# Kernel optimization log

Hardware: AMD Instinct MI355X
Metric: run time of the kernel (lower is better)

Reference implementation:

```python
import jax, jax.numpy as jnp
import numpy as np

# Longformer-base-4096 dims; attention_window=128 -> one-sided window 64
B, S, D, H, L, F, V, NUM_LABELS = 1, 4096, 768, 12, 12, 3072, 50265, 100
DH = D // H
W = 64            # one-sided sliding window
NC = S // W       # number of query chunks
EPS = 1e-5
SCALE = float(1.0 / np.sqrt(DH))


def layer_norm(x, s, b):
    m = jnp.mean(x, axis=-1, keepdims=True)
    v = jnp.mean(jnp.square(x - m), axis=-1, keepdims=True)
    return (x - m) * jax.lax.rsqrt(v + EPS) * s + b


def heads(x):  # [B,S,D] -> [B,H,S,DH]
    return x.reshape(B, S, H, DH).transpose(0, 2, 1, 3)


def chunk3(t):  # [B,H,S,DH] -> [B,H,NC,3W,DH]: key blocks c-1,c,c+1 per query chunk c
    tp = jnp.pad(t, ((0, 0), (0, 0), (W, W), (0, 0)))
    tb = tp.reshape(B, H, NC + 2, W, DH)
    return jnp.concatenate([tb[:, :, i:i + NC] for i in range(3)], axis=3)


def _forward(input_ids, attention_mask, emb_tok, emb_pos, ln_emb_scale, ln_emb_bias,
             Wq, bq, Wk, bk, Wv, bv, Wqg, bqg, Wkg, bkg, Wvg, bvg, Wo, bo,
             ln1_scale, ln1_bias, Wf1, bf1, Wf2, bf2, ln2_scale, ln2_bias, Wc, bc):
    am = attention_mask > 0                      # [B,S]
    x = layer_norm(emb_tok[input_ids] + emb_pos[None, :, :], ln_emb_scale, ln_emb_bias)

    # static sliding-window masks, shared by all layers
    qi = jnp.arange(W)[:, None]
    kj = jnp.arange(3 * W)[None, :]
    band = (kj >= qi) & (kj <= qi + 2 * W)       # |key - query| <= W within a chunk triple
    kvalid = am & (jnp.arange(S)[None, :] > 0)   # global token (pos 0) excluded from window
    kp = jnp.pad(kvalid, ((0, 0), (W, W))).reshape(B, NC + 2, W)
    kmask = jnp.concatenate([kp[:, i:i + NC] for i in range(3)], axis=2)   # [B,NC,3W]
    win_mask = band[None, None, None] & kmask[:, None, :, None, :]         # [B,1,NC,W,3W]

    def layer(x, p):
        (wq, bq_, wk, bk_, wv, bv_, wqg, bqg_, wkg, bkg_, wvg, bvg_, wo, bo_,
         l1s, l1b, wf1, bf1_, wf2, bf2_, l2s, l2b) = p
        q = heads(x @ wq + bq_) * SCALE
        k = heads(x @ wk + bk_)
        v = heads(x @ wv + bv_)
        qc = q.reshape(B, H, NC, W, DH)
        k3, v3 = chunk3(k), chunk3(v)
        sc = jnp.einsum('bhcqd,bhckd->bhcqk', qc, k3)          # [B,H,NC,W,3W]
        sc = jnp.where(win_mask, sc, -1e9)
        # every token also attends to the global CLS key (standard K/V of pos 0)
        sg = jnp.einsum('bhsd,bhd->bhs', q, k[:, :, 0]).reshape(B, H, NC, W, 1)
        probs = jax.nn.softmax(jnp.concatenate([sg, sc], axis=-1), axis=-1)
        pg, pl = probs[..., 0], probs[..., 1:]
        ctx = jnp.einsum('bhcqk,bhckd->bhcqd', pl, v3).reshape(B, H, S, DH)
        ctx = ctx + pg.reshape(B, H, S, 1) * v[:, :, :1]
        # global token attends to everything with its own (global) projections
        qg = heads(x @ wqg + bqg_)[:, :, 0] * SCALE            # [B,H,DH]
        kg = heads(x @ wkg + bkg_)
        vg = heads(x @ wvg + bvg_)
        sgl = jnp.where(am[:, None, :], jnp.einsum('bhd,bhjd->bhj', qg, kg), -1e9)
        ctx0 = jnp.einsum('bhj,bhjd->bhd', jax.nn.softmax(sgl, axis=-1), vg)
        ctx = ctx.at[:, :, 0].set(ctx0)
        attn = ctx.transpose(0, 2, 1, 3).reshape(B, S, D) @ wo + bo_
        x1 = layer_norm(x + attn, l1s, l1b)
        h = jax.nn.gelu(x1 @ wf1 + bf1_, approximate=False)
        return layer_norm(x1 + h @ wf2 + bf2_, l2s, l2b), None

    params = (Wq, bq, Wk, bk, Wv, bv, Wqg, bqg, Wkg, bkg, Wvg, bvg, Wo, bo,
              ln1_scale, ln1_bias, Wf1, bf1, Wf2, bf2, ln2_scale, ln2_bias)
    x, _ = jax.lax.scan(layer, x, params)
    return x[:, 0] @ Wc + bc                                   # [B, NUM_LABELS]


def setup_inputs():
    key = jax.random.key(0)
    ks = jax.random.split(key, 40)
    it = iter(range(40))
    nrm = lambda shape: jax.random.normal(ks[next(it)], shape, dtype=jnp.float32) * 0.02
    z = lambda shape: jnp.zeros(shape, jnp.float32)
    o = lambda shape: jnp.ones(shape, jnp.float32)
    return {
        'input_ids': jax.random.randint(ks[next(it)], (B, S), 0, V, dtype=jnp.int32),
        'attention_mask': jnp.ones((B, S), dtype=jnp.int32),
        'emb_tok': nrm((V, D)), 'emb_pos': nrm((S, D)),
        'ln_emb_scale': o((D,)), 'ln_emb_bias': z((D,)),
        'Wq': nrm((L, D, D)), 'bq': z((L, D)),
        'Wk': nrm((L, D, D)), 'bk': z((L, D)),
        'Wv': nrm((L, D, D)), 'bv': z((L, D)),
        'Wqg': nrm((L, D, D)), 'bqg': z((L, D)),
        'Wkg': nrm((L, D, D)), 'bkg': z((L, D)),
        'Wvg': nrm((L, D, D)), 'bvg': z((L, D)),
        'Wo': nrm((L, D, D)), 'bo': z((L, D)),
        'ln1_scale': o((L, D)), 'ln1_bias': z((L, D)),
        'Wf1': nrm((L, D, F)), 'bf1': z((L, F)),
        'Wf2': nrm((L, F, D)), 'bf2': z((L, D)),
        'ln2_scale': o((L, D)), 'ln2_bias': z((L, D)),
        'Wc': nrm((D, NUM_LABELS)), 'bc': z((NUM_LABELS,)),
    }


def reference(input_ids, attention_mask, emb_tok, emb_pos, ln_emb_scale, ln_emb_bias,
              Wq, bq, Wk, bk, Wv, bv, Wqg, bqg, Wkg, bkg, Wvg, bvg, Wo, bo,
              ln1_scale, ln1_bias, Wf1, bf1, Wf2, bf2, ln2_scale, ln2_bias, Wc, bc):
    return _forward(input_ids, attention_mask, emb_tok, emb_pos, ln_emb_scale, ln_emb_bias,
                    Wq, bq, Wk, bk, Wv, bv, Wqg, bqg, Wkg, bkg, Wvg, bvg, Wo, bo,
                    ln1_scale, ln1_bias, Wf1, bf1, Wf2, bf2, ln2_scale, ln2_bias, Wc, bc)
```

## Files before the change

### kernel.cpp

```cpp
#include <hip/hip_runtime.h>
#include <hip/hip_bf16.h>

typedef unsigned short u16;
typedef __attribute__((ext_vector_type(8))) short bf16x8;
typedef __attribute__((ext_vector_type(4))) float f32x4;

constexpr int S = 4096, D = 768, H = 12, NL = 12, F = 3072, NLAB = 100, DH = 64;
constexpr int NQKV = 3840;
constexpr float SCALE = 0.125f;
constexpr float EPS = 1e-5f;

__device__ __forceinline__ float bits2f(u16 u) {
  union { unsigned int i; float f; } x; x.i = ((unsigned int)u) << 16; return x.f;
}
__device__ __forceinline__ u16 f2bbits(float f) {
  union { float f; unsigned int i; } x; x.f = f;
  return (u16)((x.i + 0x7FFFu + ((x.i >> 16) & 1u)) >> 16);
}
__device__ __forceinline__ float rdw(const void* p, size_t i, int isf32) {
  return isf32 ? ((const float*)p)[i] : bits2f(((const u16*)p)[i]);
}
__device__ __forceinline__ void gload16(const void* g, void* l) {
  __builtin_amdgcn_global_load_lds(
      (const __attribute__((address_space(1))) void*)g,
      (__attribute__((address_space(3))) void*)l, 16, 0, 0);
}

__global__ void detect_k(const void* lns, int* flag) {
  *flag = (*(const unsigned int*)lns == 0x3F800000u) ? 1 : 0;
}

struct PrepArgs {
  const void *Wq, *Wk, *Wv, *Wkg, *Wvg, *Wo, *Wqg, *Wf1, *Wf2;
  const void *bq, *bk, *bv, *bkg, *bvg, *bo, *bqg, *bf1, *bf2;
  size_t oDD, oDF, oD, oF;
  u16 *wt_qkv, *wt_o, *wt_qg, *wt_f1, *wt_f2;
  float* biasb;
  const int* flag;
};

__global__ __launch_bounds__(256) void prep_layer(PrepArgs a)
{
  const int b = blockIdx.x, t = threadIdx.x;
  const int isf32 = *a.flag;
  if (b < 8640) {
    __shared__ float tile[32][33];
    const void* src; size_t soff; int N, ld, rowoff, n0, k0;
    u16* dst; float scl = 1.f;
    if (b < 4032) {
      const int m = b / 576, ti = b - m * 576;
      soff = a.oDD; N = D; ld = D; rowoff = 0;
      switch (m) {
        case 0:  src = a.Wq;  dst = a.wt_qkv; scl = SCALE;  break;
        case 1:  src = a.Wk;  dst = a.wt_qkv; rowoff = 768; break;
        case 2:  src = a.Wv;  dst = a.wt_qkv; rowoff = 1536; break;
        case 3:  src = a.Wkg; dst = a.wt_qkv; rowoff = 2304; break;
        case 4:  src = a.Wvg; dst = a.wt_qkv; rowoff = 3072; break;
        case 5:  src = a.Wo;  dst = a.wt_o;   break;
        default: src = a.Wqg; dst = a.wt_qg;  scl = SCALE;  break;
      }
      n0 = (ti % 24) * 32; k0 = (ti / 24) * 32;
    } else if (b < 6336) {
      const int ti = b - 4032;
      src = a.Wf1; soff = a.oDF; N = F; dst = a.wt_f1; rowoff = 0; ld = D;
      n0 = (ti % 96) * 32; k0 = (ti / 96) * 32;
    } else {
      const int ti = b - 6336;
      src = a.Wf2; soff = a.oDF; N = D; dst = a.wt_f2; rowoff = 0; ld = F;
      n0 = (ti % 24) * 32; k0 = (ti / 24) * 32;
    }
    const int r = t >> 3, cc = (t & 7) << 2;
    const size_t si = soff + (size_t)(k0 + r) * N + n0 + cc;
    if (isf32) {
      const float4 v = *reinterpret_cast<const float4*>(&((const float*)src)[si]);
      tile[r][cc] = v.x * scl; tile[r][cc+1] = v.y * scl;
      tile[r][cc+2] = v.z * scl; tile[r][cc+3] = v.w * scl;
    } else {
      const ushort4 v = *reinterpret_cast<const ushort4*>(&((const u16*)src)[si]);
      tile[r][cc] = bits2f(v.x) * scl; tile[r][cc+1] = bits2f(v.y) * scl;
      tile[r][cc+2] = bits2f(v.z) * scl; tile[r][cc+3] = bits2f(v.w) * scl;
    }
    __syncthreads();
    const ushort4 ov = make_ushort4(f2bbits(tile[cc+0][r]), f2bbits(tile[cc+1][r]),
                                    f2bbits(tile[cc+2][r]), f2bbits(tile[cc+3][r]));
    *reinterpret_cast<ushort4*>(&dst[(size_t)(rowoff + n0 + r) * ld + k0 + cc]) = ov;
  } else {
    const int i = (b - 8640) * 256 + t;
    float v;
    if      (i < 768)  v = rdw(a.bq,  a.oD + i,        isf32) * SCALE;
    else if (i < 1536) v = rdw(a.bk,  a.oD + i - 768,  isf32);
    else if (i < 2304) v = rdw(a.bv,  a.oD + i - 1536, isf32);
    else if (i < 3072) v = rdw(a.bkg, a.oD + i - 2304, isf32);
    else if (i < 3840) v = rdw(a.bvg, a.oD + i - 3072, isf32);
    else if (i < 4608) v = rdw(a.bo,  a.oD + i - 3840, isf32);
    else if (i < 7680) v = rdw(a.bf1, a.oF + i - 4608, isf32);
    else if (i < 8448) v = rdw(a.bf2, a.oD + i - 7680, isf32);
    else               v = rdw(a.bqg, a.oD + i - 8448, isf32) * SCALE;
    a.biasb[i] = v;
  }
}

template<int BN, int SPLITK>
__global__ __launch_bounds__(256) void mfma_gemm(
    const u16* __restrict__ A, const u16* __restrict__ BT,
    const float* __restrict__ bias,
    float* __restrict__ Cf, u16* __restrict__ Cb,
    int M, int N, int K, int act)
{
  constexpr int BM = 128, BK = 32;
  constexpr int WN = BN / 2;
  constexpr int NR = WN / 16;
  __shared__ u16 As[BM * BK];
  __shared__ u16 Bs[BN * BK];
  const int t = threadIdx.x;
  const int wid = t >> 6, lane = t & 63;
  const int wr = wid >> 1, wc = wid & 1;
  const int m0 = blockIdx.y * BM, n0 = blockIdx.x * BN;
  const int z = (SPLITK > 1) ? blockIdx.z : 0;
  const int kLen = K / SPLITK;
  const int k0 = z * kLen;
  const int l_row = lane >> 2;
  const int l_kc = (lane & 3) << 3;

  f32x4 acc[4][NR];
#pragma unroll
  for (int m = 0; m < 4; ++m)
#pragma unroll
    for (int n = 0; n < NR; ++n)
      acc[m][n] = (f32x4){0.f, 0.f, 0.f, 0.f};

  const int frow = lane & 15;
  const int fkb = (lane >> 4) << 3;

  for (int kt = k0; kt < k0 + kLen; kt += BK) {
#pragma unroll
    for (int i = 0; i < 2; ++i) {
      const int ch = wid * 2 + i;
      gload16(&A[(size_t)(m0 + ch * 16 + l_row) * K + kt + l_kc], &As[ch * 512]);
    }
#pragma unroll
    for (int i = 0; i < BN / 64; ++i) {
      const int ch = wid * (BN / 64) + i;
      gload16(&BT[(size_t)(n0 + ch * 16 + l_row) * K + kt + l_kc], &Bs[ch * 512]);
    }
    __syncthreads();
    bf16x8 af[4], bfr[NR];
#pragma unroll
    for (int m = 0; m < 4; ++m)
      af[m] = *reinterpret_cast<const bf16x8*>(&As[(wr * 64 + m * 16 + frow) * BK + fkb]);
#pragma unroll
    for (int n = 0; n < NR; ++n)
      bfr[n] = *reinterpret_cast<const bf16x8*>(&Bs[(wc * WN + n * 16 + frow) * BK + fkb]);
#pragma unroll
    for (int m = 0; m < 4; ++m)
#pragma unroll
      for (int n = 0; n < NR; ++n)
        acc[m][n] = __builtin_amdgcn_mfma_f32_16x16x32_bf16(af[m], bfr[n], acc[m][n], 0, 0, 0);
    __syncthreads();
  }

  float* Cp = (SPLITK > 1) ? (Cf + (size_t)z * M * N) : Cf;
  const int crow = (lane >> 4) << 2;
  const int ccol = lane & 15;
#pragma unroll
  for (int m = 0; m < 4; ++m) {
#pragma unroll
    for (int n = 0; n < NR; ++n) {
      const int gc = n0 + wc * WN + n * 16 + ccol;
      const float bv = (z == 0) ? bias[gc] : 0.f;
#pragma unroll
      for (int r = 0; r < 4; ++r) {
        const int gr = m0 + wr * 64 + m * 16 + crow + r;
        float x = acc[m][n][r] + bv;
        if (SPLITK == 1 && act) x = 0.5f * x * (1.0f + erff(x * 0.70710678118654752f));
        if (Cp) Cp[(size_t)gr * N + gc] = x;
        if (SPLITK == 1 && Cb) Cb[(size_t)gr * N + gc] = f2bbits(x);
      }
    }
  }
}

__global__ void embed_k(const int* __restrict__ ids, const void* __restrict__ tok,
                        const void* __restrict__ pos, float* __restrict__ out,
                        const int* __restrict__ flag)
{
  const int isf32 = *flag;
  const int s = blockIdx.x, t = threadIdx.x;
  const int id = ids[s];
  for (int c = t; c < D; c += 256)
    out[(size_t)s * D + c] = rdw(tok, (size_t)id * D + c, isf32) + rdw(pos, (size_t)s * D + c, isf32);
}

__global__ __launch_bounds__(256) void ln_res_k(
    const float* __restrict__ Ain,
    const float* __restrict__ P0, const float* __restrict__ P1,
    const float* __restrict__ P2, const float* __restrict__ P3,
    const void* __restrict__ g, size_t goff, const void* __restrict__ b, size_t boff,
    float* __restrict__ Out, u16* __restrict__ Outb, const int* __restrict__ flag)
{
  __shared__ float buf[D];
  __shared__ float red[4];
  const int isf32 = *flag;
  const int r = blockIdx.x, t = threadIdx.x;
  float ls = 0.f;
  for (int c = t; c < D; c += 256) {
    const size_t i = (size_t)r * D + c;
    float v = Ain[i];
    if (P0) v += P0[i];
    if (P1) v += P1[i];
    if (P2) v += P2[i];
    if (P3) v += P3[i];
    buf[c] = v; ls += v;
  }
#pragma unroll
  for (int off = 32; off; off >>= 1) ls += __shfl_xor(ls, off);
  if ((t & 63) == 0) red[t >> 6] = ls;
  __syncthreads();
  const float mean = (red[0] + red[1] + red[2] + red[3]) * (1.0f / D);
  __syncthreads();
  float lv = 0.f;
  for (int c = t; c < D; c += 256) { const float dd = buf[c] - mean; lv += dd * dd; }
#pragma unroll
  for (int off = 32; off; off >>= 1) lv += __shfl_xor(lv, off);
  if ((t & 63) == 0) red[t >> 6] = lv;
  __syncthreads();
  const float var = (red[0] + red[1] + red[2] + red[3]) * (1.0f / D);
  const float rstd = rsqrtf(var + EPS);
  for (int c = t; c < D; c += 256) {
    const float o = (buf[c] - mean) * rstd * rdw(g, goff + c, isf32) + rdw(b, boff + c, isf32);
    Out[(size_t)r * D + c] = o;
    if (Outb) Outb[(size_t)r * D + c] = f2bbits(o);
  }
}

__global__ __launch_bounds__(256) void qg_gemv(
    const u16* __restrict__ Xb, const u16* __restrict__ WgT,
    const float* __restrict__ biasb, float* __restrict__ QG)
{
  const int wid = threadIdx.x >> 6, lane = threadIdx.x & 63;
  const int o = blockIdx.x * 4 + wid;
  float a = 0.f;
#pragma unroll
  for (int j = 0; j < 12; ++j) {
    const int k = j * 64 + lane;
    a += bits2f(Xb[k]) * bits2f(WgT[(size_t)o * 768 + k]);
  }
#pragma unroll
  for (int off = 32; off; off >>= 1) a += __shfl_xor(a, off);
  if (lane == 0) QG[o] = a + biasb[8448 + o];
}

__global__ __launch_bounds__(256) void win_attn3(
    const u16* __restrict__ QKV, const int* __restrict__ am, u16* __restrict__ CTXb)
{
  __shared__ u16 Ql[64 * 64];
  __shared__ u16 Kl[224 * 64];
  __shared__ u16 Vt[64 * 232];
  __shared__ int kwin[224];
  const int c = blockIdx.x, h = blockIdx.y;
  const int t = threadIdx.x, w = t >> 6, lane = t & 63;
  const int base = c * 64 - 64, s0 = c * 64;

  for (int i = t; i < 1024; i += 256) {
    const int r = i >> 4, c4 = (i & 15) << 2;
    const ushort4 v = *reinterpret_cast<const ushort4*>(
        &QKV[(size_t)(s0 + r) * NQKV + h * 64 + c4]);
    *reinterpret_cast<ushort4*>((char*)Ql + ((r * 128 + c4 * 2) ^ ((r & 7) << 4))) = v;
  }
  for (int i = t; i < 3584; i += 256) {
    const int r = i >> 4, c4 = (i & 15) << 2;
    const int kp = (r < 192) ? (base + r) : ((r == 192) ? 0 : -1);
    ushort4 v = make_ushort4(0, 0, 0, 0);
    if (kp >= 0 && kp < S)
      v = *reinterpret_cast<const ushort4*>(&QKV[(size_t)kp * NQKV + 768 + h * 64 + c4]);
    *reinterpret_cast<ushort4*>((char*)Kl + ((r * 128 + c4 * 2) ^ ((r & 7) << 4))) = v;
  }
  for (int i = t; i < 3584; i += 256) {
    const int r = i >> 4, c4 = (i & 15) << 2;
    const int kp = (r < 192) ? (base + r) : ((r == 192) ? 0 : -1);
    ushort4 v = make_ushort4(0, 0, 0, 0);
    if (kp >= 0 && kp < S)
      v = *reinterpret_cast<const ushort4*>(&QKV[(size_t)kp * NQKV + 1536 + h * 64 + c4]);
    Vt[(c4 + 0) * 232 + r] = v.x;
    Vt[(c4 + 1) * 232 + r] = v.y;
    Vt[(c4 + 2) * 232 + r] = v.z;
    Vt[(c4 + 3) * 232 + r] = v.w;
  }
  if (t < 224) {
    const int kp = base + t;
    kwin[t] = (t < 192 && kp >= 1 && kp < S) ? am[kp] : 0;
  }
  __syncthreads();

  const int frow = lane & 15, fkb = (lane >> 4) << 3;
  const int crow = (lane >> 4) << 2, ccol = lane & 15;
  const int qrow = w * 16 + frow;

  bf16x8 aq[2];
#pragma unroll
  for (int ks = 0; ks < 2; ++ks)
    aq[ks] = *reinterpret_cast<const bf16x8*>(
        (const char*)Ql + ((qrow * 128 + (ks * 32 + fkb) * 2) ^ ((qrow & 7) << 4)));

  f32x4 sc[14];
#pragma unroll
  for (int tl = 0; tl < 14; ++tl) {
    sc[tl] = (f32x4){0.f, 0.f, 0.f, 0.f};
    const int key = tl * 16 + frow;
#pragma unroll
    for (int ks = 0; ks < 2; ++ks) {
      const bf16x8 bk = *reinterpret_cast<const bf16x8*>(
          (const char*)Kl + ((key * 128 + (ks * 32 + fkb) * 2) ^ ((key & 7) << 4)));
      sc[tl] = __builtin_amdgcn_mfma_f32_16x16x32_bf16(aq[ks], bk, sc[tl], 0, 0, 0);
    }
  }

  float m4[4] = {-1e30f, -1e30f, -1e30f, -1e30f};
#pragma unroll
  for (int tl = 0; tl < 14; ++tl) {
    const int kidx = tl * 16 + ccol;
    const int kw = kwin[kidx];
    const bool isg = (kidx == 192);
#pragma unroll
    for (int r = 0; r < 4; ++r) {
      const int qi = w * 16 + crow + r;
      const bool valid = isg || ((kidx >= qi) && (kidx <= qi + 128) && kw);
      const float v = valid ? sc[tl][r] : -1e30f;
      sc[tl][r] = v;
      m4[r] = fmaxf(m4[r], v);
    }
  }
#pragma unroll
  for (int r = 0; r < 4; ++r)
#pragma unroll
    for (int off = 8; off; off >>= 1) m4[r] = fmaxf(m4[r], __shfl_xor(m4[r], off));

  float ssum[4] = {0.f, 0.f, 0.f, 0.f};
#pragma unroll
  for (int tl = 0; tl < 14; ++tl)
#pragma unroll
    for (int r = 0; r < 4; ++r) {
      const float e = __expf(sc[tl][r] - m4[r]);
      sc[tl][r] = e;
      ssum[r] += e;
    }
#pragma unroll
  for (int r = 0; r < 4; ++r)
#pragma unroll
    for (int off = 8; off; off >>= 1) ssum[r] += __shfl_xor(ssum[r], off);

  __syncthreads();
  u16* Pl = Kl;
#pragma unroll
  for (int tl = 0; tl < 14; ++tl) {
    const int kidx = tl * 16 + ccol;
#pragma unroll
    for (int r = 0; r < 4; ++r) {
      const int row = crow + r;
      *(u16*)((char*)Pl + w * 7168 + ((row * 448 + kidx * 2) ^ ((row & 7) << 4))) =
          f2bbits(sc[tl][r]);
    }
  }
  __syncthreads();

  bf16x8 pa[7];
#pragma unroll
  for (int ks = 0; ks < 7; ++ks)
    pa[ks] = *reinterpret_cast<const bf16x8*>(
        (const char*)Pl + w * 7168 + ((frow * 448 + (ks * 32 + fkb) * 2) ^ ((frow & 7) << 4)));

  f32x4 av[4];
#pragma unroll
  for (int n = 0; n < 4; ++n) {
    av[n] = (f32x4){0.f, 0.f, 0.f, 0.f};
#pragma unroll
    for (int ks = 0; ks < 7; ++ks) {
      const bf16x8 bv = *reinterpret_cast<const bf16x8*>(&Vt[(n * 16 + frow) * 232 + ks * 32 + fkb]);
      av[n] = __builtin_amdgcn_mfma_f32_16x16x32_bf16(pa[ks], bv, av[n], 0, 0, 0);
    }
  }
  float inv[4];
#pragma unroll
  for (int r = 0; r < 4; ++r) inv[r] = 1.f / ssum[r];
#pragma unroll
  for (int n = 0; n < 4; ++n)
#pragma unroll
    for (int r = 0; r < 4; ++r) {
      const int s = s0 + w * 16 + crow + r;
      CTXb[(size_t)s * D + h * 64 + n * 16 + ccol] = f2bbits(av[n][r] * inv[r]);
    }
}

__global__ __launch_bounds__(256) void glob_part(
    const u16* __restrict__ QKV, const float* __restrict__ QG,
    const int* __restrict__ am, float* __restrict__ gp)
{
  __shared__ float qsh[DH];
  __shared__ float se[256];
  __shared__ float red[4];
  __shared__ float part[4][DH];
  const int seg = blockIdx.x, h = blockIdx.y, t = threadIdx.x;
  const int j0 = seg * 256;
  if (t < DH) qsh[t] = QG[h * DH + t];
  __syncthreads();
  const int j = j0 + t;
  float a = 0.f;
  const u16* kr = &QKV[(size_t)j * NQKV + 2304 + h * 64];
#pragma unroll
  for (int v8 = 0; v8 < 8; ++v8) {
    const bf16x8 kv = *reinterpret_cast<const bf16x8*>(&kr[v8 * 8]);
#pragma unroll
    for (int e = 0; e < 8; ++e)
      a += qsh[v8 * 8 + e] * bits2f((u16)kv[e]);
  }
  a = (am[j] > 0) ? a : -1e9f;
  float m = a;
#pragma unroll
  for (int off = 32; off; off >>= 1) m = fmaxf(m, __shfl_xor(m, off));
  if ((t & 63) == 0) red[t >> 6] = m;
  __syncthreads();
  m = fmaxf(fmaxf(red[0], red[1]), fmaxf(red[2], red[3]));
  const float e = __expf(a - m);
  se[t] = e;
  float ls = e;
#pragma unroll
  for (int off = 32; off; off >>= 1) ls += __shfl_xor(ls, off);
  __syncthreads();
  if ((t & 63) == 0) red[t >> 6] = ls;
  __syncthreads();
  const float lsum = red[0] + red[1] + red[2] + red[3];
  const int g = t >> 6, d = t & 63;
  float acc = 0.f;
  for (int jj = g; jj < 256; jj += 4)
    acc += se[jj] * bits2f(QKV[(size_t)(j0 + jj) * NQKV + 3072 + h * 64 + d]);
  part[g][d] = acc;
  __syncthreads();
  if (t < 64) {
    float* o = &gp[(size_t)(h * 16 + seg) * 66];
    o[t] = part[0][t] + part[1][t] + part[2][t] + part[3][t];
    if (t == 0) { o[64] = m; o[65] = lsum; }
  }
}

__global__ void glob_comb(const float* __restrict__ gp, u16* __restrict__ CTXb)
{
  const int h = blockIdx.x, t = threadIdx.x;
  float M = -1e30f;
  for (int i = 0; i < 16; ++i) M = fmaxf(M, gp[(size_t)(h * 16 + i) * 66 + 64]);
  float L = 0.f, acc = 0.f;
  for (int i = 0; i < 16; ++i) {
    const float* o = &gp[(size_t)(h * 16 + i) * 66];
    const float w = __expf(o[64] - M);
    L += o[65] * w;
    acc += o[t] * w;
  }
  CTXb[h * 64 + t] = f2bbits(acc / L);
}

__global__ __launch_bounds__(256) void cls_k(
    const float* __restrict__ X, const void* __restrict__ Wc,
    const void* __restrict__ bc, void* __restrict__ out,
    const int* __restrict__ flag)
{
  const int isf32 = *flag;
  const int wid = threadIdx.x >> 6, lane = threadIdx.x & 63;
  const int n = blockIdx.x * 4 + wid;
  if (n >= NLAB) return;
  float a = 0.f;
#pragma unroll
  for (int j = 0; j < 12; ++j) {
    const int k = j * 64 + lane;
    a += X[k] * rdw(Wc, (size_t)k * NLAB + n, isf32);
  }
#pragma unroll
  for (int off = 32; off; off >>= 1) a += __shfl_xor(a, off);
  if (lane == 0) {
    a += rdw(bc, n, isf32);
    if (isf32) ((float*)out)[n] = a;
    else ((u16*)out)[n] = f2bbits(a);
  }
}

extern "C" void kernel_launch(void* const* d_in, const int* in_sizes, int n_in,
                              void* d_out, int out_size, void* d_ws, size_t ws_size,
                              hipStream_t stream)
{
  const int*  ids = (const int*)d_in[0];
  const int*  am  = (const int*)d_in[1];
  const void* emb_tok = d_in[2];
  const void* emb_pos = d_in[3];
  const void* ln_e_g  = d_in[4];
  const void* ln_e_b  = d_in[5];
  const void* Wq  = d_in[6];  const void* bq  = d_in[7];
  const void* Wk  = d_in[8];  const void* bk  = d_in[9];
  const void* Wv  = d_in[10]; const void* bv  = d_in[11];
  const void* Wqg = d_in[12]; const void* bqg = d_in[13];
  const void* Wkg = d_in[14]; const void* bkg = d_in[15];
  const void* Wvg = d_in[16]; const void* bvg = d_in[17];
  const void* Wo  = d_in[18]; const void* bo  = d_in[19];
  const void* l1g = d_in[20]; const void* l1b = d_in[21];
  const void* Wf1 = d_in[22]; const void* bf1 = d_in[23];
  const void* Wf2 = d_in[24]; const void* bf2 = d_in[25];
  const void* l2g = d_in[26]; const void* l2b = d_in[27];
  const void* Wc  = d_in[28]; const void* bc  = d_in[29];

  float* ws = (float*)d_ws;
  const size_t SD = (size_t)S * D;
  size_t cur = 0;
  auto af32 = [&](size_t n) { float* p = ws + cur; cur += n; return p; };
  auto au16 = [&](size_t n_u16) { u16* p = (u16*)(ws + cur); cur += n_u16 / 2; return p; };

  float* X     = af32(SD);
  float* X1    = af32(SD);
  float* TMP   = af32(4 * SD);
  u16*   QKV16 = au16(5 * SD);
  u16*   Hb    = au16((size_t)S * F);
  u16*   Xb    = au16(SD);
  u16*   X1b   = au16(SD);
  u16*   CTXb  = au16(SD);
  u16*   wt_qkv = au16((size_t)NQKV * D);
  u16*   wt_o   = au16((size_t)D * D);
  u16*   wt_qg  = au16((size_t)D * D);
  u16*   wt_f1  = au16((size_t)F * D);
  u16*   wt_f2  = au16((size_t)D * F);
  float* biasb  = af32(9216);
  float* QGb    = af32(768);
  float* gp     = af32((size_t)H * 16 * 66);
  int*   flag   = (int*)af32(4);

  float* T0 = TMP;
  float* T1 = TMP + SD;
  float* T2 = TMP + 2 * SD;
  float* T3 = TMP + 3 * SD;

  detect_k<<<1, 1, 0, stream>>>(ln_e_g, flag);
  embed_k<<<S, 256, 0, stream>>>(ids, emb_tok, emb_pos, T0, flag);
  ln_res_k<<<S, 256, 0, stream>>>(T0, nullptr, nullptr, nullptr, nullptr,
                                  ln_e_g, 0, ln_e_b, 0, X, Xb, flag);

  for (int l = 0; l < NL; ++l) {
    PrepArgs pa;
    pa.Wq = Wq; pa.Wk = Wk; pa.Wv = Wv; pa.Wkg = Wkg; pa.Wvg = Wvg;
    pa.Wo = Wo; pa.Wqg = Wqg; pa.Wf1 = Wf1; pa.Wf2 = Wf2;
    pa.bq = bq; pa.bk = bk; pa.bv = bv; pa.bkg = bkg; pa.bvg = bvg;
    pa.bo = bo; pa.bqg = bqg; pa.bf1 = bf1; pa.bf2 = bf2;
    pa.oDD = (size_t)l * D * D; pa.oDF = (size_t)l * D * F;
    pa.oD = (size_t)l * D; pa.oF = (size_t)l * F;
    pa.wt_qkv = wt_qkv; pa.wt_o = wt_o; pa.wt_qg = wt_qg;
    pa.wt_f1 = wt_f1; pa.wt_f2 = wt_f2; pa.biasb = biasb; pa.flag = flag;
    prep_layer<<<8676, 256, 0, stream>>>(pa);

    mfma_gemm<128, 1><<<dim3(NQKV / 128, S / 128), 256, 0, stream>>>(
        Xb, wt_qkv, biasb, nullptr, QKV16, S, NQKV, D, 0);
    qg_gemv<<<192, 256, 0, stream>>>(Xb, wt_qg, biasb, QGb);
    win_attn3<<<dim3(S / 64, H), 256, 0, stream>>>(QKV16, am, CTXb);
    glob_part<<<dim3(16, H), 256, 0, stream>>>(QKV16, QGb, am, gp);
    glob_comb<<<H, 64, 0, stream>>>(gp, CTXb);
    mfma_gemm<64, 2><<<dim3(D / 64, S / 128, 2), 256, 0, stream>>>(
        CTXb, wt_o, biasb + 3840, TMP, nullptr, S, D, D, 0);
    ln_res_k<<<S, 256, 0, stream>>>(X, T0, T1, nullptr, nullptr,
                                    l1g, pa.oD, l1b, pa.oD, X1, X1b, flag);
    mfma_gemm<128, 1><<<dim3(F / 128, S / 128), 256, 0, stream>>>(
        X1b, wt_f1, biasb + 4608, nullptr, Hb, S, F, D, 1);
    mfma_gemm<64, 4><<<dim3(D / 64, S / 128, 4), 256, 0, stream>>>(
        Hb, wt_f2, biasb + 7680, TMP, nullptr, S, D, F, 0);
    ln_res_k<<<S, 256, 0, stream>>>(X1, T0, T1, T2, T3,
                                    l2g, pa.oD, l2b, pa.oD, X, Xb, flag);
  }
  cls_k<<<25, 256, 0, stream>>>(X, Wc, bc, d_out, flag);
}
```

Measured before the change: 3.182 ms.

## Batch weight prep, use warp-per-row layernorm, halve FFN2 split-K

All twelve layers' weight transposes and bias packing now run in one prep launch before the layer loop, with per-layer slices of larger workspace buffers, instead of one prep launch per layer. The residual-plus-layernorm kernel now handles one row per wavefront with float4 loads held in registers, which drops shared memory and block-wide barriers. The FFN2 GEMM split-K drops from 4 to 2, so it writes and re-reads two fewer partial-sum buffers. The trade-offs are more workspace memory and fewer blocks for the FFN2 GEMM.

```diff
diff --git a/kernel.cpp b/kernel.cpp
--- a/kernel.cpp
+++ b/kernel.cpp
@@ -33,40 +33,50 @@
 struct PrepArgs {
   const void *Wq, *Wk, *Wv, *Wkg, *Wvg, *Wo, *Wqg, *Wf1, *Wf2;
   const void *bq, *bk, *bv, *bkg, *bvg, *bo, *bqg, *bf1, *bf2;
-  size_t oDD, oDF, oD, oF;
   u16 *wt_qkv, *wt_o, *wt_qg, *wt_f1, *wt_f2;
   float* biasb;
   const int* flag;
 };
 
-__global__ __launch_bounds__(256) void prep_layer(PrepArgs a)
-{
-  const int b = blockIdx.x, t = threadIdx.x;
+__global__ __launch_bounds__(256) void prep_all(PrepArgs a)
+{
+  const int l = blockIdx.x / 8676;
+  const int b = blockIdx.x % 8676;
+  const int t = threadIdx.x;
   const int isf32 = *a.flag;
+  const size_t oDD = (size_t)l * D * D, oDF = (size_t)l * D * F;
+  const size_t oD = (size_t)l * D, oF = (size_t)l * F;
+  u16* wqkv = a.wt_qkv + (size_t)l * NQKV * D;
+  u16* wo   = a.wt_o   + (size_t)l * D * D;
+  u16* wqg  = a.wt_qg  + (size_t)l * D * D;
+  u16* wf1  = a.wt_f1  + (size_t)l * F * D;
+  u16* wf2  = a.wt_f2  + (size_t)l * D * F;
+  float* bb = a.biasb + (size_t)l * 9216;
+
   if (b < 8640) {
     __shared__ float tile[32][33];
     const void* src; size_t soff; int N, ld, rowoff, n0, k0;
     u16* dst; float scl = 1.f;
     if (b < 4032) {
       const int m = b / 576, ti = b - m * 576;
-      soff = a.oDD; N = D; ld = D; rowoff = 0;
+      soff = oDD; N = D; ld = D; rowoff = 0;
       switch (m) {
-        case 0:  src = a.Wq;  dst = a.wt_qkv; scl = SCALE;  break;
-        case 1:  src = a.Wk;  dst = a.wt_qkv; rowoff = 768; break;
-        case 2:  src = a.Wv;  dst = a.wt_qkv; rowoff = 1536; break;
-        case 3:  src = a.Wkg; dst = a.wt_qkv; rowoff = 2304; break;
-        case 4:  src = a.Wvg; dst = a.wt_qkv; rowoff = 3072; break;
-        case 5:  src = a.Wo;  dst = a.wt_o;   break;
-        default: src = a.Wqg; dst = a.wt_qg;  scl = SCALE;  break;
+        case 0:  src = a.Wq;  dst = wqkv; scl = SCALE;  break;
+        case 1:  src = a.Wk;  dst = wqkv; rowoff = 768; break;
+        case 2:  src = a.Wv;  dst = wqkv; rowoff = 1536; break;
+        case 3:  src = a.Wkg; dst = wqkv; rowoff = 2304; break;
+        case 4:  src = a.Wvg; dst = wqkv; rowoff = 3072; break;
+        case 5:  src = a.Wo;  dst = wo;   break;
+        default: src = a.Wqg; dst = wqg;  scl = SCALE;  break;
       }
       n0 = (ti % 24) * 32; k0 = (ti / 24) * 32;
     } else if (b < 6336) {
       const int ti = b - 4032;
-      src = a.Wf1; soff = a.oDF; N = F; dst = a.wt_f1; rowoff = 0; ld = D;
+      src = a.Wf1; soff = oDF; N = F; dst = wf1; rowoff = 0; ld = D;
       n0 = (ti % 96) * 32; k0 = (ti / 96) * 32;
     } else {
       const int ti = b - 6336;
-      src = a.Wf2; soff = a.oDF; N = D; dst = a.wt_f2; rowoff = 0; ld = F;
+      src = a.Wf2; soff = oDF; N = D; dst = wf2; rowoff = 0; ld = F;
       n0 = (ti % 24) * 32; k0 = (ti / 24) * 32;
     }
     const int r = t >> 3, cc = (t & 7) << 2;
@@ -87,16 +97,16 @@
   } else {
     const int i = (b - 8640) * 256 + t;
     float v;
-    if      (i < 768)  v = rdw(a.bq,  a.oD + i,        isf32) * SCALE;
-    else if (i < 1536) v = rdw(a.bk,  a.oD + i - 768,  isf32);
-    else if (i < 2304) v = rdw(a.bv,  a.oD + i - 1536, isf32);
-    else if (i < 3072) v = rdw(a.bkg, a.oD + i - 2304, isf32);
-    else if (i < 3840) v = rdw(a.bvg, a.oD + i - 3072, isf32);
-    else if (i < 4608) v = rdw(a.bo,  a.oD + i - 3840, isf32);
-    else if (i < 7680) v = rdw(a.bf1, a.oF + i - 4608, isf32);
-    else if (i < 8448) v = rdw(a.bf2, a.oD + i - 7680, isf32);
-    else               v = rdw(a.bqg, a.oD + i - 8448, isf32) * SCALE;
-    a.biasb[i] = v;
+    if      (i < 768)  v = rdw(a.bq,  oD + i,        isf32) * SCALE;
+    else if (i < 1536) v = rdw(a.bk,  oD + i - 768,  isf32);
+    else if (i < 2304) v = rdw(a.bv,  oD + i - 1536, isf32);
+    else if (i < 3072) v = rdw(a.bkg, oD + i - 2304, isf32);
+    else if (i < 3840) v = rdw(a.bvg, oD + i - 3072, isf32);
+    else if (i < 4608) v = rdw(a.bo,  oD + i - 3840, isf32);
+    else if (i < 7680) v = rdw(a.bf1, oF + i - 4608, isf32);
+    else if (i < 8448) v = rdw(a.bf2, oD + i - 7680, isf32);
+    else               v = rdw(a.bqg, oD + i - 8448, isf32) * SCALE;
+    bb[i] = v;
   }
 }
 
@@ -198,38 +208,47 @@
     const void* __restrict__ g, size_t goff, const void* __restrict__ b, size_t boff,
     float* __restrict__ Out, u16* __restrict__ Outb, const int* __restrict__ flag)
 {
-  __shared__ float buf[D];
-  __shared__ float red[4];
   const int isf32 = *flag;
-  const int r = blockIdx.x, t = threadIdx.x;
+  const int w = threadIdx.x >> 6, lane = threadIdx.x & 63;
+  const int r = blockIdx.x * 4 + w;
+  const size_t rb = (size_t)r * D;
+  float v[12];
   float ls = 0.f;
-  for (int c = t; c < D; c += 256) {
-    const size_t i = (size_t)r * D + c;
-    float v = Ain[i];
-    if (P0) v += P0[i];
-    if (P1) v += P1[i];
-    if (P2) v += P2[i];
-    if (P3) v += P3[i];
-    buf[c] = v; ls += v;
+#pragma unroll
+  for (int j = 0; j < 3; ++j) {
+    const int c = lane * 4 + j * 256;
+    float4 x = *reinterpret_cast<const float4*>(&Ain[rb + c]);
+    if (P0) { const float4 p = *reinterpret_cast<const float4*>(&P0[rb + c]);
+              x.x += p.x; x.y += p.y; x.z += p.z; x.w += p.w; }
+    if (P1) { const float4 p = *reinterpret_cast<const float4*>(&P1[rb + c]);
+              x.x += p.x; x.y += p.y; x.z += p.z; x.w += p.w; }
+    if (P2) { const float4 p = *reinterpret_cast<const float4*>(&P2[rb + c]);
+              x.x += p.x; x.y += p.y; x.z += p.z; x.w += p.w; }
+    if (P3) { const float4 p = *reinterpret_cast<const float4*>(&P3[rb + c]);
+              x.x += p.x; x.y += p.y; x.z += p.z; x.w += p.w; }
+    v[j*4+0] = x.x; v[j*4+1] = x.y; v[j*4+2] = x.z; v[j*4+3] = x.w;
+    ls += x.x + x.y + x.z + x.w;
   }
 #pragma unroll
   for (int off = 32; off; off >>= 1) ls += __shfl_xor(ls, off);
-  if ((t & 63) == 0) red[t >> 6] = ls;
-  __syncthreads();
-  const float mean = (red[0] + red[1] + red[2] + red[3]) * (1.0f / D);
-  __syncthreads();
+  const float mean = ls * (1.0f / D);
   float lv = 0.f;
-  for (int c = t; c < D; c += 256) { const float dd = buf[c] - mean; lv += dd * dd; }
+#pragma unroll
+  for (int e = 0; e < 12; ++e) { const float dd = v[e] - mean; lv += dd * dd; }
 #pragma unroll
   for (int off = 32; off; off >>= 1) lv += __shfl_xor(lv, off);
-  if ((t & 63) == 0) red[t >> 6] = lv;
-  __syncthreads();
-  const float var = (red[0] + red[1] + red[2] + red[3]) * (1.0f / D);
-  const float rstd = rsqrtf(var + EPS);
-  for (int c = t; c < D; c += 256) {
-    const float o = (buf[c] - mean) * rstd * rdw(g, goff + c, isf32) + rdw(b, boff + c, isf32);
-    Out[(size_t)r * D + c] = o;
-    if (Outb) Outb[(size_t)r * D + c] = f2bbits(o);
+  const float rstd = rsqrtf(lv * (1.0f / D) + EPS);
+#pragma unroll
+  for (int j = 0; j < 3; ++j) {
+    const int c = lane * 4 + j * 256;
+    float o[4];
+#pragma unroll
+    for (int e = 0; e < 4; ++e)
+      o[e] = (v[j*4+e] - mean) * rstd * rdw(g, goff + c + e, isf32) + rdw(b, boff + c + e, isf32);
+    *reinterpret_cast<float4*>(&Out[rb + c]) = make_float4(o[0], o[1], o[2], o[3]);
+    if (Outb)
+      *reinterpret_cast<ushort4*>(&Outb[rb + c]) =
+          make_ushort4(f2bbits(o[0]), f2bbits(o[1]), f2bbits(o[2]), f2bbits(o[3]));
   }
 }
 
@@ -508,64 +527,69 @@
   const size_t SD = (size_t)S * D;
   size_t cur = 0;
   auto af32 = [&](size_t n) { float* p = ws + cur; cur += n; return p; };
-  auto au16 = [&](size_t n_u16) { u16* p = (u16*)(ws + cur); cur += n_u16 / 2; return p; };
+  auto au16 = [&](size_t n_u16) { u16* p = (u16*)(ws + cur); cur += (n_u16 + 1) / 2; return p; };
 
   float* X     = af32(SD);
   float* X1    = af32(SD);
-  float* TMP   = af32(4 * SD);
+  float* TMP   = af32(2 * SD);
   u16*   QKV16 = au16(5 * SD);
   u16*   Hb    = au16((size_t)S * F);
   u16*   Xb    = au16(SD);
   u16*   X1b   = au16(SD);
   u16*   CTXb  = au16(SD);
-  u16*   wt_qkv = au16((size_t)NQKV * D);
-  u16*   wt_o   = au16((size_t)D * D);
-  u16*   wt_qg  = au16((size_t)D * D);
-  u16*   wt_f1  = au16((size_t)F * D);
-  u16*   wt_f2  = au16((size_t)D * F);
-  float* biasb  = af32(9216);
+  u16*   wt_qkv = au16((size_t)NL * NQKV * D);
+  u16*   wt_o   = au16((size_t)NL * D * D);
+  u16*   wt_qg  = au16((size_t)NL * D * D);
+  u16*   wt_f1  = au16((size_t)NL * F * D);
+  u16*   wt_f2  = au16((size_t)NL * D * F);
+  float* biasb  = af32((size_t)NL * 9216);
   float* QGb    = af32(768);
   float* gp     = af32((size_t)H * 16 * 66);
   int*   flag   = (int*)af32(4);
 
   float* T0 = TMP;
   float* T1 = TMP + SD;
-  float* T2 = TMP + 2 * SD;
-  float* T3 = TMP + 3 * SD;
 
   detect_k<<<1, 1, 0, stream>>>(ln_e_g, flag);
+
+  PrepArgs pa;
+  pa.Wq = Wq; pa.Wk = Wk; pa.Wv = Wv; pa.Wkg = Wkg; pa.Wvg = Wvg;
+  pa.Wo = Wo; pa.Wqg = Wqg; pa.Wf1 = Wf1; pa.Wf2 = Wf2;
+  pa.bq = bq; pa.bk = bk; pa.bv = bv; pa.bkg = bkg; pa.bvg = bvg;
+  pa.bo = bo; pa.bqg = bqg; pa.bf1 = bf1; pa.bf2 = bf2;
+  pa.wt_qkv = wt_qkv; pa.wt_o = wt_o; pa.wt_qg = wt_qg;
+  pa.wt_f1 = wt_f1; pa.wt_f2 = wt_f2; pa.biasb = biasb; pa.flag = flag;
+  prep_all<<<NL * 8676, 256, 0, stream>>>(pa);
+
   embed_k<<<S, 256, 0, stream>>>(ids, emb_tok, emb_pos, T0, flag);
-  ln_res_k<<<S, 256, 0, stream>>>(T0, nullptr, nullptr, nullptr, nullptr,
-                                  ln_e_g, 0, ln_e_b, 0, X, Xb, flag);
+  ln_res_k<<<S / 4, 256, 0, stream>>>(T0, nullptr, nullptr, nullptr, nullptr,
+                                      ln_e_g, 0, ln_e_b, 0, X, Xb, flag);
 
   for (int l = 0; l < NL; ++l) {
-    PrepArgs pa;
-    pa.Wq = Wq; pa.Wk = Wk; pa.Wv = Wv; pa.Wkg = Wkg; pa.Wvg = Wvg;
-    pa.Wo = Wo; pa.Wqg = Wqg; pa.Wf1 = Wf1; pa.Wf2 = Wf2;
-    pa.bq = bq; pa.bk = bk; pa.bv = bv; pa.bkg = bkg; pa.bvg = bvg;
-    pa.bo = bo; pa.bqg = bqg; pa.bf1 = bf1; pa.bf2 = bf2;
-    pa.oDD = (size_t)l * D * D; pa.oDF = (size_t)l * D * F;
-    pa.oD = (size_t)l * D; pa.oF = (size_t)l * F;
-    pa.wt_qkv = wt_qkv; pa.wt_o = wt_o; pa.wt_qg = wt_qg;
-    pa.wt_f1 = wt_f1; pa.wt_f2 = wt_f2; pa.biasb = biasb; pa.flag = flag;
-    prep_layer<<<8676, 256, 0, stream>>>(pa);
+    const size_t oD = (size_t)l * D;
+    u16* wqkv_l = wt_qkv + (size_t)l * NQKV * D;
+    u16* wo_l   = wt_o   + (size_t)l * D * D;
+    u16* wqg_l  = wt_qg  + (size_t)l * D * D;
+    u16* wf1_l  = wt_f1  + (size_t)l * F * D;
+    u16* wf2_l  = wt_f2  + (size_t)l * D * F;
+    float* bb_l = biasb + (size_t)l * 9216;
 
     mfma_gemm<128, 1><<<dim3(NQKV / 128, S / 128), 256, 0, stream>>>(
-        Xb, wt_qkv, biasb, nullptr, QKV16, S, NQKV, D, 0);
-    qg_gemv<<<192, 256, 0, stream>>>(Xb, wt_qg, biasb, QGb);
+        Xb, wqkv_l, bb_l, nullptr, QKV16, S, NQKV, D, 0);
+    qg_gemv<<<192, 256, 0, stream>>>(Xb, wqg_l, bb_l, QGb);
     win_attn3<<<dim3(S / 64, H), 256, 0, stream>>>(QKV16, am, CTXb);
     glob_part<<<dim3(16, H), 256, 0, stream>>>(QKV16, QGb, am, gp);
     glob_comb<<<H, 64, 0, stream>>>(gp, CTXb);
     mfma_gemm<64, 2><<<dim3(D / 64, S / 128, 2), 256, 0, stream>>>(
-        CTXb, wt_o, biasb + 3840, TMP, nullptr, S, D, D, 0);
-    ln_res_k<<<S, 256, 0, stream>>>(X, T0, T1, nullptr, nullptr,
-                                    l1g, pa.oD, l1b, pa.oD, X1, X1b, flag);
+        CTXb, wo_l, bb_l + 3840, TMP, nullptr, S, D, D, 0);
+    ln_res_k<<<S / 4, 256, 0, stream>>>(X, T0, T1, nullptr, nullptr,
+                                        l1g, oD, l1b, oD, X1, X1b, flag);
     mfma_gemm<128, 1><<<dim3(F / 128, S / 128), 256, 0, stream>>>(
-        X1b, wt_f1, biasb + 4608, nullptr, Hb, S, F, D, 1);
-    mfma_gemm<64, 4><<<dim3(D / 64, S / 128, 4), 256, 0, stream>>>(
-        Hb, wt_f2, biasb + 7680, TMP, nullptr, S, D, F, 0);
-    ln_res_k<<<S, 256, 0, stream>>>(X1, T0, T1, T2, T3,
-                                    l2g, pa.oD, l2b, pa.oD, X, Xb, flag);
+        X1b, wf1_l, bb_l + 4608, nullptr, Hb, S, F, D, 1);
+    mfma_gemm<64, 2><<<dim3(D / 64, S / 128, 2), 256, 0, stream>>>(
+        Hb, wf2_l, bb_l + 7680, TMP, nullptr, S, D, F, 0);
+    ln_res_k<<<S / 4, 256, 0, stream>>>(X1, T0, T1, nullptr, nullptr,
+                                        l2g, oD, l2b, oD, X, Xb, flag);
   }
   cls_k<<<25, 256, 0, stream>>>(X, Wc, bc, d_out, flag);
 }
```

Measured after the change: 3.104 ms. 1.02x faster.
